# Kernel tuning notes

Measured on AMD Instinct MI355X. Metric: run time of the kernel, lower is better.

## Reference

```python
import jax, jax.numpy as jnp
import numpy as np

B, C, H, W = 4, 16, 512, 512


def setup_inputs() -> dict:
    key = jax.random.key(0)
    k1, k2, k3, k4, k5 = jax.random.split(key, 5)
    # positive depth in [0.5, 10.5] meters
    depth = jax.random.uniform(k1, (B, 1, H, W), dtype=jnp.float32) * 10.0 + 0.5
    # realistic, well-conditioned camera intrinsics per batch element
    fx = 500.0 + 20.0 * jax.random.normal(k2, (B,), dtype=jnp.float32)
    fy = 500.0 + 20.0 * jax.random.normal(k3, (B,), dtype=jnp.float32)
    zeros = jnp.zeros((B,), jnp.float32)
    ones = jnp.ones((B,), jnp.float32)
    K = jnp.stack([
        jnp.stack([fx, zeros, ones * (W / 2.0)], axis=-1),
        jnp.stack([zeros, fy, ones * (H / 2.0)], axis=-1),
        jnp.stack([zeros, zeros, ones], axis=-1),
    ], axis=1)  # [B,3,3]
    # near-identity rigid-ish transforms so homogeneous w ~ 1
    T = jnp.eye(4, dtype=jnp.float32)[None, None] + 0.05 * jax.random.normal(k4, (B, C, 4, 4), dtype=jnp.float32)
    masks = jax.random.randint(k5, (B, C, H, W), 0, 2).astype(jnp.bool_)
    return {"depth": depth, "K": K, "T": T, "masks": masks}


def reference(depth, K, T, masks):
    b, _, h, w = depth.shape
    c = masks.shape[1]
    n = h * w
    eps = 1e-10
    # --- depth -> point cloud ---
    u = jnp.arange(w, dtype=depth.dtype)
    v = jnp.arange(h, dtype=depth.dtype)
    uu, vv = jnp.meshgrid(u, v, indexing='xy')            # [H,W]
    uv1 = jnp.stack([uu, vv, jnp.ones_like(uu)], axis=-1)  # [H,W,3]
    K_inv = jnp.linalg.inv(K)                              # [B,3,3]
    d = jnp.transpose(depth, (0, 2, 3, 1))                 # [B,H,W,1]
    points_3d = jnp.einsum('bij,hwj->bhwi', K_inv, uv1) * d  # [B,H,W,3]
    # --- per-object masked transform (vectorized over all channels) ---
    pts = points_3d.reshape(b, n, 3)
    pts_h = jnp.concatenate([pts, jnp.ones((b, n, 1), pts.dtype)], axis=-1)  # [B,N,4]
    trans_h = jnp.einsum('bcij,bnj->bcni', T, pts_h)       # [B,C,N,4]
    trans3 = trans_h[..., :3] / (trans_h[..., 3:] + eps)   # [B,C,N,3]
    masks_flat = masks.reshape(b, c, n)
    out = pts
    for ci in range(c):
        out = jnp.where(masks_flat[:, ci, :, None], trans3[:, ci], out)
    tp = out.reshape(b, h, w, 3)                           # transformed points
    # --- reproject to depth map (scatter) ---
    p2h = jnp.einsum('bij,bhwj->bhwi', K, tp)              # [B,H,W,3]
    p2 = p2h[..., :2] / (p2h[..., 2:] + eps)
    Z = tp[..., 2]                                         # [B,H,W]
    u_idx = jnp.clip(p2[..., 0], 0, w - 1).astype(jnp.int32)
    v_idx = jnp.clip(p2[..., 1], 0, h - 1).astype(jnp.int32)
    b_idx = jnp.broadcast_to(jnp.arange(b)[:, None, None], (b, h, w))
    depth_map = depth.at[b_idx, 0, v_idx, u_idx].set(Z)
    return depth_map
```

## Files before the change

### kernel.cpp

```cpp
#include <hip/hip_runtime.h>
#include <stdint.h>

constexpr int B = 4, C = 16, H = 512, W = 512;
constexpr int N = H * W;
constexpr int BLOCKS_PER_BATCH = N / 256;
constexpr int NXCD = 8;
constexpr float EPS = 1e-10f;


__device__ __forceinline__ void swizzle_bn(int orig, int tid, int& b, int& n) {
    int xcd = orig & (NXCD - 1);
    int j   = orig >> 3;
    b       = j >> 7;
    int r   = j & 127;
    int blk = xcd * 128 + r;
    n = (blk << 8) + tid;
}

__global__ __launch_bounds__(256) void project_atomic_kernel(
    const float* __restrict__ depth,
    const float* __restrict__ K,
    const float* __restrict__ T,
    const int*   __restrict__ masks,
    unsigned*    __restrict__ keys,
    float*       __restrict__ zplane)
{
    __shared__ float Ts[16][17];

    int b, n;
    swizzle_bn(blockIdx.x, threadIdx.x, b, n);
    int idx = b * N + n;
    int v = n >> 9;
    int u = n & (W - 1);
    int lane = threadIdx.x & 63;

    float d = depth[idx];
    const int* mb = masks + (size_t)b * C * N + n;
    int m[16];
    #pragma unroll
    for (int c = 0; c < 16; ++c) m[c] = mb[(size_t)c * N];

    {
        int t = threadIdx.x;
        int c = t >> 4, e = t & 15;
        Ts[e][c] = T[(size_t)b * 256 + t];
    }
    __syncthreads();

    const float* Kb = K + b * 9;
    float k00 = Kb[0], k01 = Kb[1], k02 = Kb[2];
    float k10 = Kb[3], k11 = Kb[4], k12 = Kb[5];
    float k20 = Kb[6], k21 = Kb[7], k22 = Kb[8];

    float c00 =  (k11 * k22 - k12 * k21);
    float c01 = -(k10 * k22 - k12 * k20);
    float c02 =  (k10 * k21 - k11 * k20);
    float det = k00 * c00 + k01 * c01 + k02 * c02;
    float invdet = 1.0f / det;
    float i00 =  (k11 * k22 - k12 * k21) * invdet;
    float i01 = -(k01 * k22 - k02 * k21) * invdet;
    float i02 =  (k01 * k12 - k02 * k11) * invdet;
    float i10 = -(k10 * k22 - k12 * k20) * invdet;
    float i11 =  (k00 * k22 - k02 * k20) * invdet;
    float i12 = -(k00 * k12 - k02 * k10) * invdet;
    float i20 =  (k10 * k21 - k11 * k20) * invdet;
    float i21 = -(k00 * k21 - k01 * k20) * invdet;
    float i22 =  (k00 * k11 - k01 * k10) * invdet;

    float uf = (float)u, vf = (float)v;
    float px = (i00 * uf + i01 * vf + i02) * d;
    float py = (i10 * uf + i11 * vf + i12) * d;
    float pz = (i20 * uf + i21 * vf + i22) * d;

    unsigned bm = 0;
    #pragma unroll
    for (int c = 0; c < 16; ++c) bm |= (m[c] ? 1u : 0u) << c;
    int sel = bm ? (31 - __clz(bm)) : -1;

    float ox = px, oy = py, oz = pz;
    if (sel >= 0) {
        float tx = Ts[0][sel]  * px + Ts[1][sel]  * py + Ts[2][sel]  * pz + Ts[3][sel];
        float ty = Ts[4][sel]  * px + Ts[5][sel]  * py + Ts[6][sel]  * pz + Ts[7][sel];
        float tz = Ts[8][sel]  * px + Ts[9][sel]  * py + Ts[10][sel] * pz + Ts[11][sel];
        float tw = Ts[12][sel] * px + Ts[13][sel] * py + Ts[14][sel] * pz + Ts[15][sel];
        float denom = tw + EPS;
        ox = tx / denom;
        oy = ty / denom;
        oz = tz / denom;
    }

    zplane[idx] = oz;

    float qx = k00 * ox + k01 * oy + k02 * oz;
    float qy = k10 * ox + k11 * oy + k12 * oz;
    float qz = k20 * ox + k21 * oy + k22 * oz;
    float zz = qz + EPS;
    float pu = qx / zz;
    float pv = qy / zz;
    pu = fminf(fmaxf(pu, 0.0f), (float)(W - 1));
    pv = fminf(fmaxf(pv, 0.0f), (float)(H - 1));
    int ui = (int)pu;
    int vi = (int)pv;
    unsigned t = (unsigned)(vi * W + ui);

    bool dom = false;
    #pragma unroll
    for (int delta = 1; delta <= 4; ++delta) {
        unsigned tn = (unsigned)__shfl_down((int)t, delta);
        dom |= (lane + delta < 64) && (tn == t);
    }
    if (!dom) {
        atomicMin(&keys[(size_t)b * N + t], (unsigned)(N - 1 - n));
    }
}

__global__ __launch_bounds__(256) void resolve_kernel(
    const unsigned* __restrict__ keys,
    const float*    __restrict__ zplane,
    const float*    __restrict__ depth,
    float*          __restrict__ out)
{
    int idx = blockIdx.x * blockDim.x + threadIdx.x;
    if (idx >= B * N) return;
    int b = idx >> 18;
    unsigned k = keys[idx];
    if (k <= (unsigned)(N - 1)) {
        int n_w = N - 1 - (int)k;
        out[idx] = zplane[(size_t)b * N + n_w];
    } else {
        out[idx] = depth[idx];
    }
}

extern "C" void kernel_launch(void* const* d_in, const int* in_sizes, int n_in,
                              void* d_out, int out_size, void* d_ws, size_t ws_size,
                              hipStream_t stream) {
    const float* depth = (const float*)d_in[0];
    const float* K     = (const float*)d_in[1];
    const float* T     = (const float*)d_in[2];
    const int*   masks = (const int*)d_in[3];
    float* out = (float*)d_out;

    char* ws = (char*)d_ws;
    unsigned* keys  = (unsigned*)ws;
    float* zplane   = (float*)(ws + (size_t)B * N * 4);

    int grid = B * BLOCKS_PER_BATCH;
    project_atomic_kernel<<<grid, 256, 0, stream>>>(depth, K, T, masks, keys, zplane);
    resolve_kernel<<<grid, 256, 0, stream>>>(keys, zplane, depth, out);
}
```

Baseline: 130.8 us.

## Process four pixels per thread with vectorized loads and adjacent-only dedup

```diff
diff --git a/kernel.cpp b/kernel.cpp
--- a/kernel.cpp
+++ b/kernel.cpp
@@ -3,18 +3,18 @@
 
 constexpr int B = 4, C = 16, H = 512, W = 512;
 constexpr int N = H * W;
-constexpr int BLOCKS_PER_BATCH = N / 256;
+constexpr int PPT = 4;
+constexpr int BLOCKS_PER_BATCH = N / (256 * PPT);
 constexpr int NXCD = 8;
 constexpr float EPS = 1e-10f;
 
 
-__device__ __forceinline__ void swizzle_bn(int orig, int tid, int& b, int& n) {
+__device__ __forceinline__ void swizzle_bn(int orig, int& b, int& blk) {
     int xcd = orig & (NXCD - 1);
     int j   = orig >> 3;
-    b       = j >> 7;
-    int r   = j & 127;
-    int blk = xcd * 128 + r;
-    n = (blk << 8) + tid;
+    b       = j >> 5;
+    int r   = j & 31;
+    blk     = xcd * 32 + r;
 }
 
 __global__ __launch_bounds__(256) void project_atomic_kernel(
@@ -27,18 +27,20 @@
 {
     __shared__ float Ts[16][17];
 
-    int b, n;
-    swizzle_bn(blockIdx.x, threadIdx.x, b, n);
-    int idx = b * N + n;
-    int v = n >> 9;
-    int u = n & (W - 1);
+    int b, blk;
+    swizzle_bn(blockIdx.x, b, blk);
+    int n0 = blk * 1024 + threadIdx.x * PPT;
+    int idx0 = b * N + n0;
+    int v = n0 >> 9;
+    int u0 = n0 & (W - 1);
     int lane = threadIdx.x & 63;
 
-    float d = depth[idx];
-    const int* mb = masks + (size_t)b * C * N + n;
-    int m[16];
+    float4 d4 = *reinterpret_cast<const float4*>(depth + idx0);
+    const int* mb = masks + (size_t)b * C * N + n0;
+    int4 m4[16];
     #pragma unroll
-    for (int c = 0; c < 16; ++c) m[c] = mb[(size_t)c * N];
+    for (int c = 0; c < 16; ++c)
+        m4[c] = *reinterpret_cast<const int4*>(mb + (size_t)c * N);
 
     {
         int t = threadIdx.x;
@@ -67,50 +69,67 @@
     float i21 = -(k00 * k21 - k01 * k20) * invdet;
     float i22 =  (k00 * k11 - k01 * k10) * invdet;
 
-    float uf = (float)u, vf = (float)v;
-    float px = (i00 * uf + i01 * vf + i02) * d;
-    float py = (i10 * uf + i11 * vf + i12) * d;
-    float pz = (i20 * uf + i21 * vf + i22) * d;
+    float vf = (float)v;
+    float ax = i01 * vf + i02;
+    float ay = i11 * vf + i12;
+    float az = i21 * vf + i22;
 
-    unsigned bm = 0;
+    unsigned tgt[PPT];
+    float    zout[PPT];
+
     #pragma unroll
-    for (int c = 0; c < 16; ++c) bm |= (m[c] ? 1u : 0u) << c;
-    int sel = bm ? (31 - __clz(bm)) : -1;
+    for (int j = 0; j < PPT; ++j) {
+        float d  = (j == 0) ? d4.x : (j == 1) ? d4.y : (j == 2) ? d4.z : d4.w;
+        float uf = (float)(u0 + j);
+        float px = (i00 * uf + ax) * d;
+        float py = (i10 * uf + ay) * d;
+        float pz = (i20 * uf + az) * d;
 
-    float ox = px, oy = py, oz = pz;
-    if (sel >= 0) {
-        float tx = Ts[0][sel]  * px + Ts[1][sel]  * py + Ts[2][sel]  * pz + Ts[3][sel];
-        float ty = Ts[4][sel]  * px + Ts[5][sel]  * py + Ts[6][sel]  * pz + Ts[7][sel];
-        float tz = Ts[8][sel]  * px + Ts[9][sel]  * py + Ts[10][sel] * pz + Ts[11][sel];
-        float tw = Ts[12][sel] * px + Ts[13][sel] * py + Ts[14][sel] * pz + Ts[15][sel];
-        float denom = tw + EPS;
-        ox = tx / denom;
-        oy = ty / denom;
-        oz = tz / denom;
+        unsigned bm = 0;
+        #pragma unroll
+        for (int c = 0; c < 16; ++c) {
+            int mc = (j == 0) ? m4[c].x : (j == 1) ? m4[c].y
+                   : (j == 2) ? m4[c].z : m4[c].w;
+            bm |= (mc ? 1u : 0u) << c;
+        }
+        int sel = bm ? (31 - __clz(bm)) : -1;
+
+        float ox = px, oy = py, oz = pz;
+        if (sel >= 0) {
+            float tx = Ts[0][sel]*px + Ts[1][sel]*py + Ts[2][sel]*pz + Ts[3][sel];
+            float ty = Ts[4][sel]*px + Ts[5][sel]*py + Ts[6][sel]*pz + Ts[7][sel];
+            float tz = Ts[8][sel]*px + Ts[9][sel]*py + Ts[10][sel]*pz + Ts[11][sel];
+            float tw = Ts[12][sel]*px + Ts[13][sel]*py + Ts[14][sel]*pz + Ts[15][sel];
+            float denom = tw + EPS;
+            ox = tx / denom;
+            oy = ty / denom;
+            oz = tz / denom;
+        }
+        zout[j] = oz;
+
+        float qx = k00 * ox + k01 * oy + k02 * oz;
+        float qy = k10 * ox + k11 * oy + k12 * oz;
+        float qz = k20 * ox + k21 * oy + k22 * oz;
+        float zz = qz + EPS;
+        float pu = qx / zz;
+        float pv = qy / zz;
+        pu = fminf(fmaxf(pu, 0.0f), (float)(W - 1));
+        pv = fminf(fmaxf(pv, 0.0f), (float)(H - 1));
+        tgt[j] = (unsigned)((int)pv * W + (int)pu);
     }
 
-    zplane[idx] = oz;
+    *reinterpret_cast<float4*>(zplane + idx0) =
+        make_float4(zout[0], zout[1], zout[2], zout[3]);
 
-    float qx = k00 * ox + k01 * oy + k02 * oz;
-    float qy = k10 * ox + k11 * oy + k12 * oz;
-    float qz = k20 * ox + k21 * oy + k22 * oz;
-    float zz = qz + EPS;
-    float pu = qx / zz;
-    float pv = qy / zz;
-    pu = fminf(fmaxf(pu, 0.0f), (float)(W - 1));
-    pv = fminf(fmaxf(pv, 0.0f), (float)(H - 1));
-    int ui = (int)pu;
-    int vi = (int)pv;
-    unsigned t = (unsigned)(vi * W + ui);
-
-    bool dom = false;
+    unsigned tnext0 = (unsigned)__shfl_down((int)tgt[0], 1);
     #pragma unroll
-    for (int delta = 1; delta <= 4; ++delta) {
-        unsigned tn = (unsigned)__shfl_down((int)t, delta);
-        dom |= (lane + delta < 64) && (tn == t);
-    }
-    if (!dom) {
-        atomicMin(&keys[(size_t)b * N + t], (unsigned)(N - 1 - n));
+    for (int j = 0; j < PPT; ++j) {
+        unsigned tn = (j < PPT - 1) ? tgt[j + 1]
+                    : (lane < 63 ? tnext0 : 0xFFFFFFFFu);
+        if (tgt[j] != tn) {
+            atomicMin(&keys[(size_t)b * N + tgt[j]],
+                      (unsigned)(N - 1 - (n0 + j)));
+        }
     }
 }
 
@@ -147,5 +166,5 @@
 
     int grid = B * BLOCKS_PER_BATCH;
     project_atomic_kernel<<<grid, 256, 0, stream>>>(depth, K, T, masks, keys, zplane);
-    resolve_kernel<<<grid, 256, 0, stream>>>(keys, zplane, depth, out);
+    resolve_kernel<<<B * N / 256, 256, 0, stream>>>(keys, zplane, depth, out);
 }
```

After: 142.6 us. 9.0% more time.
